# Kernel optimization log

Measured on AMD Instinct MI355X. Metric: run time of the kernel, lower is better.

## Reference

```python
import jax, jax.numpy as jnp
import numpy as np

B, S, D, H = 2, 2048, 1024, 16
HD = D // H  # 64

def _make_freqs():
    # flux-style rotation matrices: [1,1,S,HD//2,2,2]
    theta = 10000.0
    inv = 1.0 / (theta ** (np.arange(0, HD, 2, dtype=np.float32) / HD))  # [HD//2]
    pos = np.arange(S, dtype=np.float32)
    ang = pos[:, None] * inv[None, :]  # [S, HD//2]
    cos, sin = np.cos(ang), np.sin(ang)
    rot = np.stack([np.stack([cos, -sin], -1), np.stack([sin, cos], -1)], -2)  # [S,HD//2,2,2]
    return jnp.asarray(rot[None, None], dtype=jnp.float32)

def setup_inputs() -> dict:
    key = jax.random.key(0)
    ks = jax.random.split(key, 9)
    sc = 1.0 / np.sqrt(D)
    return {
        "x": jax.random.normal(ks[0], (B, S, D), jnp.float32),
        "freqs": _make_freqs(),
        "Wq": jax.random.normal(ks[1], (D, D), jnp.float32) * sc,
        "bq": jax.random.normal(ks[2], (D,), jnp.float32) * 0.01,
        "Wk": jax.random.normal(ks[3], (D, D), jnp.float32) * sc,
        "bk": jax.random.normal(ks[4], (D,), jnp.float32) * 0.01,
        "Wv": jax.random.normal(ks[5], (D, D), jnp.float32) * sc,
        "bv": jax.random.normal(ks[6], (D,), jnp.float32) * 0.01,
        "Wo": jax.random.normal(ks[7], (D, D), jnp.float32) * sc,
        "bo": jax.random.normal(ks[8], (D,), jnp.float32) * 0.01,
    }

def _apply_rope(xq, xk, freqs):
    # xq/xk: [B,H,S,HD]; freqs: [1,1,S,HD//2,2,2]
    def rot(t):
        t_ = t.reshape(*t.shape[:-1], -1, 1, 2)  # [B,H,S,HD//2,1,2]
        out = freqs[..., 0] * t_[..., 0] + freqs[..., 1] * t_[..., 1]  # [B,H,S,HD//2,2]
        return out.reshape(t.shape).astype(t.dtype)
    return rot(xq), rot(xk)

def reference(x, freqs, Wq, bq, Wk, bk, Wv, bv, Wo, bo):
    b, s, _ = x.shape
    # QKV projections (torch Linear: x @ W.T + b)
    q = (x @ Wq.T + bq).reshape(b, s, H, HD).transpose(0, 2, 1, 3)  # [B,H,S,HD]
    k = (x @ Wk.T + bk).reshape(b, s, H, HD).transpose(0, 2, 1, 3)
    v = (x @ Wv.T + bv).reshape(b, s, H, HD).transpose(0, 2, 1, 3)
    q, k = _apply_rope(q, k, freqs)
    # scaled dot product attention, no mask, no dropout
    scale = 1.0 / jnp.sqrt(jnp.asarray(HD, x.dtype))
    scores = jnp.einsum("bhqd,bhkd->bhqk", q, k) * scale
    attn = jax.nn.softmax(scores, axis=-1)
    o = jnp.einsum("bhqk,bhkd->bhqd", attn, v)  # [B,H,S,HD]
    o = o.transpose(0, 2, 1, 3).reshape(b, s, D)
    return o @ Wo.T + bo
```

## Files before the change

kernel.cpp:

```cpp
#include <hip/hip_runtime.h>
#include <cmath>

#define B_ 2
#define S_ 2048
#define D_ 1024
#define H_ 16
#define HD_ 64
#define M_ 4096

typedef __attribute__((ext_vector_type(8))) short short8;
typedef __attribute__((ext_vector_type(4))) short short4v;
typedef __attribute__((ext_vector_type(4))) float f32x4;

__device__ __forceinline__ short f2bf(float x) {
    unsigned u = __builtin_bit_cast(unsigned, x);
    u += 0x7fffu + ((u >> 16) & 1u);
    return (short)(u >> 16);
}

__device__ __forceinline__ void gload_lds16(const short* g, short* l) {
    __builtin_amdgcn_global_load_lds(
        (const __attribute__((address_space(1))) unsigned int*)g,
        (__attribute__((address_space(3))) unsigned int*)l, 16, 0, 0);
}

__global__ __launch_bounds__(256) void cast_all_kernel(
    const float* __restrict__ x,  const float* __restrict__ Wq,
    const float* __restrict__ Wk, const float* __restrict__ Wv,
    const float* __restrict__ Wo,
    short* __restrict__ xb, short* __restrict__ Wqkvb, short* __restrict__ Wob)
{
    const size_t i = (size_t)blockIdx.x * 256 + threadIdx.x;
    const float* src; short* dst; size_t off;
    if (i < 1048576)      { src = x;  dst = xb;              off = i; }
    else if (i < 1310720) { src = Wq; dst = Wqkvb;           off = i - 1048576; }
    else if (i < 1572864) { src = Wk; dst = Wqkvb + 1048576; off = i - 1310720; }
    else if (i < 1835008) { src = Wv; dst = Wqkvb + 2097152; off = i - 1572864; }
    else                  { src = Wo; dst = Wob;             off = i - 1835008; }
    float4 v = ((const float4*)src)[off];
    short4v o = { f2bf(v.x), f2bf(v.y), f2bf(v.z), f2bf(v.w) };
    ((short4v*)dst)[off] = o;
}

template<int MODE, int TM, int TN>
__global__ __launch_bounds__(256) void gemm_db(
    const short* __restrict__ A, const short* __restrict__ Bw,
    const float* __restrict__ b0p, const float* __restrict__ b1p, const float* __restrict__ b2p,
    const float* __restrict__ freqs,
    void* __restrict__ out0, void* __restrict__ out1, void* __restrict__ out2)
{
    constexpr int RT = TM / 32, CT = TN / 32;
    __shared__ __align__(16) short A0[TM*32];
    __shared__ __align__(16) short A1[TM*32];
    __shared__ __align__(16) short Bs0[TN*32];
    __shared__ __align__(16) short Bs1[TN*32];
    const int t = threadIdx.x;
    const int w = t >> 6;
    const int lane = t & 63;
    const int qd = lane >> 4, l = lane & 15;
    const int n0 = blockIdx.x * TN, m0 = blockIdx.y * TM;
    const int wr = (w >> 1) * (TM/2), wc = (w & 1) * (TN/2);
    const int srow  = lane >> 2;
    const int sslot = ((lane & 3) ^ ((lane >> 3) & 3)) * 8;
    const int rsw = (l >> 1) & 3;

    f32x4 acc[RT][CT] = {};

    auto STAGE = [&](int k0, short* As, short* Bss) {
        #pragma unroll
        for (int j = 0; j < TM/64; ++j) {
            const int r0 = (j*4 + w) * 16;
            gload_lds16(A + (size_t)(m0 + r0 + srow)*1024 + k0 + sslot, &As[r0*32]);
        }
        #pragma unroll
        for (int j = 0; j < TN/64; ++j) {
            const int r0 = (j*4 + w) * 16;
            gload_lds16(Bw + (size_t)(n0 + r0 + srow)*1024 + k0 + sslot, &Bss[r0*32]);
        }
    };

    auto COMP = [&](const short* As, const short* Bss) {
        short8 af[RT], bfr[CT];
        #pragma unroll
        for (int rt = 0; rt < RT; ++rt)
            af[rt] = *(const short8*)&As[(wr + rt*16 + l)*32 + ((qd ^ rsw) << 3)];
        #pragma unroll
        for (int ct = 0; ct < CT; ++ct)
            bfr[ct] = *(const short8*)&Bss[(wc + ct*16 + l)*32 + ((qd ^ rsw) << 3)];
        #pragma unroll
        for (int rt = 0; rt < RT; ++rt)
            #pragma unroll
            for (int ct = 0; ct < CT; ++ct)
                acc[rt][ct] = __builtin_amdgcn_mfma_f32_16x16x32_bf16(af[rt], bfr[ct], acc[rt][ct], 0, 0, 0);
    };

    STAGE(0, A0, Bs0);
    __syncthreads();
    for (int p = 0; p < 16; ++p) {
        STAGE((2*p + 1)*32, A1, Bs1);
        COMP(A0, Bs0);
        __syncthreads();
        if (p < 15)
            STAGE((2*p + 2)*32, A0, Bs0);
        COMP(A1, Bs1);
        __syncthreads();
    }

    if (MODE == 0) {
        float* out = (float*)out0;
        #pragma unroll
        for (int rt = 0; rt < RT; ++rt)
            #pragma unroll
            for (int ct = 0; ct < CT; ++ct) {
                const int n = n0 + wc + ct*16 + l;
                const float bias = b0p[n];
                #pragma unroll
                for (int r = 0; r < 4; ++r) {
                    const int m = m0 + wr + rt*16 + qd*4 + r;
                    out[(size_t)m*1024 + n] = acc[rt][ct][r] + bias;
                }
            }
    } else {
        const int sel = n0 >> 10;
        const int nb = n0 & 1023;
        const float* bias = (sel == 0) ? b0p : (sel == 1) ? b1p : b2p;
        if (sel < 2) {
            short* outg = (short*)((sel == 0) ? out0 : out1);
            #pragma unroll
            for (int rt = 0; rt < RT; ++rt)
                #pragma unroll
                for (int ct = 0; ct < CT; ++ct) {
                    const int d = nb + wc + ct*16 + l;
                    const float bsv = bias[d];
                    const int h = d >> 6, hd = d & 63;
                    #pragma unroll
                    for (int r = 0; r < 4; ++r) {
                        const int m = m0 + wr + rt*16 + qd*4 + r;
                        const int bb = m >> 11, s = m & 2047;
                        float val = acc[rt][ct][r] + bsv;
                        float pv = __shfl_xor(val, 1);
                        const float* f = freqs + (size_t)s*128 + (size_t)(hd >> 1)*4;
                        float o = (d & 1) ? (f[2]*pv + f[3]*val) : (f[0]*val + f[1]*pv);
                        outg[((size_t)(bb*16 + h)*2048 + s)*64 + hd] = f2bf(o);
                    }
                }
        } else {
            short* outv = (short*)out2;
            #pragma unroll
            for (int rt = 0; rt < RT; ++rt)
                #pragma unroll
                for (int ct = 0; ct < CT; ++ct) {
                    const int d = nb + wc + ct*16 + l;
                    const float bsv = bias[d];
                    const int h = d >> 6, hd = d & 63;
                    const int m0r = m0 + wr + rt*16 + qd*4;
                    const int bb = m0r >> 11, s0 = m0r & 2047;
                    short4v pk;
                    #pragma unroll
                    for (int r = 0; r < 4; ++r) pk[r] = f2bf(acc[rt][ct][r] + bsv);
                    *(short4v*)&outv[((size_t)(bb*16 + h)*64 + hd)*2048 + s0] = pk;
                }
        }
    }
}

__global__ __launch_bounds__(512) void attn_mfma(
    const short* __restrict__ qg, const short* __restrict__ kg,
    const short* __restrict__ vtg, short* __restrict__ og)
{
    __shared__ __align__(16) short K0[64*64];
    __shared__ __align__(16) short K1[64*64];
    __shared__ __align__(16) short V0[64*64];
    __shared__ __align__(16) short V1[64*64];
    __shared__ __align__(16) short Pb[128*64];

    const int t = threadIdx.x;
    const int w = t >> 6;
    const int lane = t & 63;
    const int qd = lane >> 4, l = lane & 15;
    const int l7 = lane & 7;
    const int q0 = blockIdx.x * 128;
    const int bh = blockIdx.y;

    const int rl  = lane >> 3;
    const int ss8 = ((lane & 7) ^ rl) << 3;

    short8 qf[2];
    const short* qb = qg + ((size_t)bh*2048 + q0 + w*16)*64;
    #pragma unroll
    for (int kf = 0; kf < 2; ++kf)
        qf[kf] = *(const short8*)&qb[l*64 + kf*32 + qd*8];

    f32x4 oacc[4] = {};
    float lsum = 0.f;

    const short* kbase = kg  + (size_t)bh*2048*64;
    const short* vbase = vtg + (size_t)bh*64*2048;
    const float SC = 0.125f * 1.44269504088896340736f;

    auto PREF = [&](int c, short* Kd, short* Vd) {
        gload_lds16(kbase + (size_t)(c*64 + w*8 + rl)*64 + ss8,   &Kd[(w*8)*64]);
        gload_lds16(vbase + (size_t)(w*8 + rl)*2048 + c*64 + ss8, &Vd[(w*8)*64]);
    };

    auto TILE = [&](const short* Kc, const short* Vc) {
        f32x4 sacc[4] = {};
        #pragma unroll
        for (int ct = 0; ct < 4; ++ct) {
            short8 k0f = *(const short8*)&Kc[(ct*16 + l)*64 + (((0 + qd) ^ l7) << 3)];
            short8 k1f = *(const short8*)&Kc[(ct*16 + l)*64 + (((4 + qd) ^ l7) << 3)];
            sacc[ct] = __builtin_amdgcn_mfma_f32_16x16x32_bf16(k0f, qf[0], sacc[ct], 0, 0, 0);
            sacc[ct] = __builtin_amdgcn_mfma_f32_16x16x32_bf16(k1f, qf[1], sacc[ct], 0, 0, 0);
        }
        #pragma unroll
        for (int ct = 0; ct < 4; ++ct) {
            float p0 = exp2f(sacc[ct][0] * SC);
            float p1 = exp2f(sacc[ct][1] * SC);
            float p2 = exp2f(sacc[ct][2] * SC);
            float p3 = exp2f(sacc[ct][3] * SC);
            lsum += (p0 + p1) + (p2 + p3);
            union { unsigned u[2]; short4v s; } cv;
            asm("v_cvt_pk_bf16_f32 %0, %1, %2" : "=v"(cv.u[0]) : "v"(p0), "v"(p1));
            asm("v_cvt_pk_bf16_f32 %0, %1, %2" : "=v"(cv.u[1]) : "v"(p2), "v"(p3));
            *(short4v*)&Pb[(w*16 + l)*64 + (((ct*32 + qd*8) ^ (l7 << 4)) >> 1)] = cv.s;
        }
        #pragma unroll
        for (int kf = 0; kf < 2; ++kf) {
            const int so = ((kf*4 + qd) ^ l7) << 3;
            short8 pa = *(const short8*)&Pb[(w*16 + l)*64 + so];
            #pragma unroll
            for (int ht = 0; ht < 4; ++ht) {
                short8 vb = *(const short8*)&Vc[(ht*16 + l)*64 + so];
                oacc[ht] = __builtin_amdgcn_mfma_f32_16x16x32_bf16(pa, vb, oacc[ht], 0, 0, 0);
            }
        }
    };

    PREF(0, K0, V0);
    __syncthreads();
    for (int p = 0; p < 16; ++p) {
        PREF(2*p + 1, K1, V1);
        TILE(K0, V0);
        __syncthreads();
        if (p < 15)
            PREF(2*p + 2, K0, V0);
        TILE(K1, V1);
        __syncthreads();
    }

    lsum += __shfl_xor(lsum, 16);
    lsum += __shfl_xor(lsum, 32);
    float inv[4];
    #pragma unroll
    for (int r = 0; r < 4; ++r)
        inv[r] = 1.0f / __shfl(lsum, qd*4 + r);

    const int bb = bh >> 4, h = bh & 15;
    #pragma unroll
    for (int ht = 0; ht < 4; ++ht)
        #pragma unroll
        for (int r = 0; r < 4; ++r) {
            const int s = q0 + w*16 + qd*4 + r;
            og[((size_t)bb*2048 + s)*1024 + h*64 + ht*16 + l] =
                f2bf(oacc[ht][r] * inv[r]);
        }
}

extern "C" void kernel_launch(void* const* d_in, const int* in_sizes, int n_in,
                              void* d_out, int out_size, void* d_ws, size_t ws_size,
                              hipStream_t stream)
{
    const float* x  = (const float*)d_in[0];
    const float* fr = (const float*)d_in[1];
    const float* Wq = (const float*)d_in[2];
    const float* bq = (const float*)d_in[3];
    const float* Wk = (const float*)d_in[4];
    const float* bk = (const float*)d_in[5];
    const float* Wv = (const float*)d_in[6];
    const float* bv = (const float*)d_in[7];
    const float* Wo = (const float*)d_in[8];
    const float* bo = (const float*)d_in[9];
    float* out = (float*)d_out;

    short* ws    = (short*)d_ws;
    short* xb    = ws;
    short* Wqkvb = xb    + 4194304;
    short* Wob   = Wqkvb + 3145728;
    short* qg    = Wob   + 1048576;
    short* kg    = qg    + 4194304;
    short* vtg   = kg    + 4194304;
    short* og    = vtg   + 4194304;

    cast_all_kernel<<<8192, 256, 0, stream>>>(x, Wq, Wk, Wv, Wo, xb, Wqkvb, Wob);
    gemm_db<1,128,128><<<dim3(24, 32), 256, 0, stream>>>(xb, Wqkvb, bq, bk, bv, fr, qg, kg, vtg);
    attn_mfma<<<dim3(16, 32), 512, 0, stream>>>(qg, kg, vtg, og);
    gemm_db<0,64,64><<<dim3(16, 64), 256, 0, stream>>>(og, Wob, bo, nullptr, nullptr, nullptr,
                                                       out, nullptr, nullptr);
}
```

Measured before the change: 247.7 us.

## Replace syncthreads with vmcnt-based waits to keep two stages in flight

The double-buffered loops in the GEMM and attention kernels now issue loads for two tiles up front. Each stage then waits with explicit s_waitcnt vmcnt(N) plus a raw barrier, so the next tile's global-to-LDS loads stay outstanding while the current tile is computed, instead of draining at every __syncthreads. The output projection GEMM tile also grows from 64x64 to 128x64, halving its grid. The hand-counted vmcnt values must match the number of loads issued per STAGE/PREF, otherwise the kernel races.

```diff
diff --git a/kernel.cpp b/kernel.cpp
--- a/kernel.cpp
+++ b/kernel.cpp
@@ -23,6 +23,15 @@
         (const __attribute__((address_space(1))) unsigned int*)g,
         (__attribute__((address_space(3))) unsigned int*)l, 16, 0, 0);
 }
+
+template<int N> __device__ __forceinline__ void vwait() {
+    if constexpr (N == 0) asm volatile("s_waitcnt vmcnt(0)" ::: "memory");
+    else if constexpr (N == 2) asm volatile("s_waitcnt vmcnt(2)" ::: "memory");
+    else if constexpr (N == 3) asm volatile("s_waitcnt vmcnt(3)" ::: "memory");
+    else if constexpr (N == 4) asm volatile("s_waitcnt vmcnt(4)" ::: "memory");
+}
+__device__ __forceinline__ void lgwait0() { asm volatile("s_waitcnt lgkmcnt(0)" ::: "memory"); }
+__device__ __forceinline__ void bar() { __builtin_amdgcn_s_barrier(); }
 
 __global__ __launch_bounds__(256) void cast_all_kernel(
     const float* __restrict__ x,  const float* __restrict__ Wq,
@@ -50,6 +59,7 @@
     void* __restrict__ out0, void* __restrict__ out1, void* __restrict__ out2)
 {
     constexpr int RT = TM / 32, CT = TN / 32;
+    constexpr int LPC = TM/64 + TN/64;
     __shared__ __align__(16) short A0[TM*32];
     __shared__ __align__(16) short A1[TM*32];
     __shared__ __align__(16) short Bs0[TN*32];
@@ -95,16 +105,21 @@
     };
 
     STAGE(0, A0, Bs0);
-    __syncthreads();
-    for (int p = 0; p < 16; ++p) {
-        STAGE((2*p + 1)*32, A1, Bs1);
+    STAGE(32, A1, Bs1);
+    for (int p = 0; p < 30; p += 2) {
+        vwait<LPC>(); bar();
         COMP(A0, Bs0);
-        __syncthreads();
-        if (p < 15)
-            STAGE((2*p + 2)*32, A0, Bs0);
+        lgwait0(); bar();
+        STAGE((p + 2)*32, A0, Bs0);
+        vwait<LPC>(); bar();
         COMP(A1, Bs1);
-        __syncthreads();
+        lgwait0(); bar();
+        STAGE((p + 3)*32, A1, Bs1);
     }
+    vwait<LPC>(); bar();
+    COMP(A0, Bs0);
+    vwait<0>(); bar();
+    COMP(A1, Bs1);
 
     if (MODE == 0) {
         float* out = (float*)out0;
@@ -237,16 +252,21 @@
     };
 
     PREF(0, K0, V0);
-    __syncthreads();
-    for (int p = 0; p < 16; ++p) {
-        PREF(2*p + 1, K1, V1);
+    PREF(1, K1, V1);
+    for (int p = 0; p < 30; p += 2) {
+        vwait<2>(); bar();
         TILE(K0, V0);
-        __syncthreads();
-        if (p < 15)
-            PREF(2*p + 2, K0, V0);
+        lgwait0(); bar();
+        PREF(p + 2, K0, V0);
+        vwait<2>(); bar();
         TILE(K1, V1);
-        __syncthreads();
+        lgwait0(); bar();
+        PREF(p + 3, K1, V1);
     }
+    vwait<2>(); bar();
+    TILE(K0, V0);
+    vwait<0>(); bar();
+    TILE(K1, V1);
 
     lsum += __shfl_xor(lsum, 16);
     lsum += __shfl_xor(lsum, 32);
@@ -294,6 +314,6 @@
     cast_all_kernel<<<8192, 256, 0, stream>>>(x, Wq, Wk, Wv, Wo, xb, Wqkvb, Wob);
     gemm_db<1,128,128><<<dim3(24, 32), 256, 0, stream>>>(xb, Wqkvb, bq, bk, bv, fr, qg, kg, vtg);
     attn_mfma<<<dim3(16, 32), 512, 0, stream>>>(qg, kg, vtg, og);
-    gemm_db<0,64,64><<<dim3(16, 64), 256, 0, stream>>>(og, Wob, bo, nullptr, nullptr, nullptr,
-                                                       out, nullptr, nullptr);
-}
+    gemm_db<0,128,64><<<dim3(16, 32), 256, 0, stream>>>(og, Wob, bo, nullptr, nullptr, nullptr,
+                                                        out, nullptr, nullptr);
+}
```

Result: no change. 251.8 us (+1.6%).

## Double K-step per stage in GEMMs with 8-way XOR swizzle and explicit waits

Applied to the files above, without the earlier changes.

Each pipeline stage of both projection GEMMs now covers a K chunk of 64 instead of 32, which halves the number of barrier phases. The LDS layout uses rows of 64 elements with an 8-slot XOR swizzle. Syncthreads is replaced by an explicit vmcnt(0) wait plus s_barrier. The output projection tile grows from 64x64 to 128x64, which improves operand reuse but halves the grid size and doubles LDS use per block.

```diff
diff --git a/kernel.cpp b/kernel.cpp
--- a/kernel.cpp
+++ b/kernel.cpp
@@ -23,6 +23,9 @@
         (const __attribute__((address_space(1))) unsigned int*)g,
         (__attribute__((address_space(3))) unsigned int*)l, 16, 0, 0);
 }
+
+__device__ __forceinline__ void vwait0() { asm volatile("s_waitcnt vmcnt(0)" ::: "memory"); }
+__device__ __forceinline__ void bar()    { __builtin_amdgcn_s_barrier(); }
 
 __global__ __launch_bounds__(256) void cast_all_kernel(
     const float* __restrict__ x,  const float* __restrict__ Wq,
@@ -43,67 +46,70 @@
 }
 
 template<int MODE, int TM, int TN>
-__global__ __launch_bounds__(256) void gemm_db(
+__global__ __launch_bounds__(256) void gemm_2ph(
     const short* __restrict__ A, const short* __restrict__ Bw,
     const float* __restrict__ b0p, const float* __restrict__ b1p, const float* __restrict__ b2p,
     const float* __restrict__ freqs,
     void* __restrict__ out0, void* __restrict__ out1, void* __restrict__ out2)
 {
     constexpr int RT = TM / 32, CT = TN / 32;
-    __shared__ __align__(16) short A0[TM*32];
-    __shared__ __align__(16) short A1[TM*32];
-    __shared__ __align__(16) short Bs0[TN*32];
-    __shared__ __align__(16) short Bs1[TN*32];
+    __shared__ __align__(16) short A0[TM*64];
+    __shared__ __align__(16) short A1[TM*64];
+    __shared__ __align__(16) short Bs0[TN*64];
+    __shared__ __align__(16) short Bs1[TN*64];
     const int t = threadIdx.x;
     const int w = t >> 6;
     const int lane = t & 63;
     const int qd = lane >> 4, l = lane & 15;
+    const int l7 = lane & 7;
     const int n0 = blockIdx.x * TN, m0 = blockIdx.y * TM;
     const int wr = (w >> 1) * (TM/2), wc = (w & 1) * (TN/2);
-    const int srow  = lane >> 2;
-    const int sslot = ((lane & 3) ^ ((lane >> 3) & 3)) * 8;
-    const int rsw = (l >> 1) & 3;
+    const int rl  = lane >> 3;
+    const int ss8 = ((lane & 7) ^ rl) << 3;
 
     f32x4 acc[RT][CT] = {};
 
     auto STAGE = [&](int k0, short* As, short* Bss) {
         #pragma unroll
-        for (int j = 0; j < TM/64; ++j) {
-            const int r0 = (j*4 + w) * 16;
-            gload_lds16(A + (size_t)(m0 + r0 + srow)*1024 + k0 + sslot, &As[r0*32]);
-        }
-        #pragma unroll
-        for (int j = 0; j < TN/64; ++j) {
-            const int r0 = (j*4 + w) * 16;
-            gload_lds16(Bw + (size_t)(n0 + r0 + srow)*1024 + k0 + sslot, &Bss[r0*32]);
+        for (int j = 0; j < TM/32; ++j) {
+            const int r0 = (j*4 + w) * 8;
+            gload_lds16(A + (size_t)(m0 + r0 + rl)*1024 + k0 + ss8, &As[r0*64]);
+        }
+        #pragma unroll
+        for (int j = 0; j < TN/32; ++j) {
+            const int r0 = (j*4 + w) * 8;
+            gload_lds16(Bw + (size_t)(n0 + r0 + rl)*1024 + k0 + ss8, &Bss[r0*64]);
         }
     };
 
     auto COMP = [&](const short* As, const short* Bss) {
-        short8 af[RT], bfr[CT];
-        #pragma unroll
-        for (int rt = 0; rt < RT; ++rt)
-            af[rt] = *(const short8*)&As[(wr + rt*16 + l)*32 + ((qd ^ rsw) << 3)];
-        #pragma unroll
-        for (int ct = 0; ct < CT; ++ct)
-            bfr[ct] = *(const short8*)&Bss[(wc + ct*16 + l)*32 + ((qd ^ rsw) << 3)];
-        #pragma unroll
-        for (int rt = 0; rt < RT; ++rt)
+        #pragma unroll
+        for (int kk = 0; kk < 2; ++kk) {
+            short8 af[RT], bfr[CT];
+            #pragma unroll
+            for (int rt = 0; rt < RT; ++rt)
+                af[rt] = *(const short8*)&As[(wr + rt*16 + l)*64 + (((kk*4 + qd) ^ l7) << 3)];
             #pragma unroll
             for (int ct = 0; ct < CT; ++ct)
-                acc[rt][ct] = __builtin_amdgcn_mfma_f32_16x16x32_bf16(af[rt], bfr[ct], acc[rt][ct], 0, 0, 0);
+                bfr[ct] = *(const short8*)&Bss[(wc + ct*16 + l)*64 + (((kk*4 + qd) ^ l7) << 3)];
+            #pragma unroll
+            for (int rt = 0; rt < RT; ++rt)
+                #pragma unroll
+                for (int ct = 0; ct < CT; ++ct)
+                    acc[rt][ct] = __builtin_amdgcn_mfma_f32_16x16x32_bf16(af[rt], bfr[ct], acc[rt][ct], 0, 0, 0);
+        }
     };
 
     STAGE(0, A0, Bs0);
-    __syncthreads();
-    for (int p = 0; p < 16; ++p) {
-        STAGE((2*p + 1)*32, A1, Bs1);
+    vwait0(); bar();
+    for (int p = 0; p < 16; p += 2) {
+        STAGE((p + 1)*64, A1, Bs1);
         COMP(A0, Bs0);
-        __syncthreads();
-        if (p < 15)
-            STAGE((2*p + 2)*32, A0, Bs0);
+        vwait0(); bar();
+        if (p + 2 < 16)
+            STAGE((p + 2)*64, A0, Bs0);
         COMP(A1, Bs1);
-        __syncthreads();
+        vwait0(); bar();
     }
 
     if (MODE == 0) {
@@ -292,8 +298,8 @@
     short* og    = vtg   + 4194304;
 
     cast_all_kernel<<<8192, 256, 0, stream>>>(x, Wq, Wk, Wv, Wo, xb, Wqkvb, Wob);
-    gemm_db<1,128,128><<<dim3(24, 32), 256, 0, stream>>>(xb, Wqkvb, bq, bk, bv, fr, qg, kg, vtg);
+    gemm_2ph<1,128,128><<<dim3(24, 32), 256, 0, stream>>>(xb, Wqkvb, bq, bk, bv, fr, qg, kg, vtg);
     attn_mfma<<<dim3(16, 32), 512, 0, stream>>>(qg, kg, vtg, og);
-    gemm_db<0,64,64><<<dim3(16, 64), 256, 0, stream>>>(og, Wob, bo, nullptr, nullptr, nullptr,
-                                                       out, nullptr, nullptr);
-}
+    gemm_2ph<0,128,64><<<dim3(16, 32), 256, 0, stream>>>(og, Wob, bo, nullptr, nullptr, nullptr,
+                                                         out, nullptr, nullptr);
+}
```

Result: slower. 278.5 us (+12.4%).

## Triple-buffer GEMM LDS staging with explicit vmcnt waits and barriers

Applied to the files above, without the earlier changes.

Replaces the double-buffered GEMM main loop with a three-stage LDS ring. Each step waits only on the oldest outstanding global-to-LDS loads (s_waitcnt vmcnt) and issues a raw s_barrier, instead of a full __syncthreads drain. This keeps two K-chunks of loads in flight while the MFMA work runs, hiding more global memory latency. The cost is 50% more shared memory per block, which may reduce occupancy. It also relies on hand-counted wait values, which must match the number of load instructions each stage issues.

```diff
diff --git a/kernel.cpp b/kernel.cpp
--- a/kernel.cpp
+++ b/kernel.cpp
@@ -23,6 +23,17 @@
         (const __attribute__((address_space(1))) unsigned int*)g,
         (__attribute__((address_space(3))) unsigned int*)l, 16, 0, 0);
 }
+
+template<int N> __device__ __forceinline__ void vwait() {
+    if constexpr (N == 0) asm volatile("s_waitcnt vmcnt(0)" ::: "memory");
+    else if constexpr (N == 2) asm volatile("s_waitcnt vmcnt(2)" ::: "memory");
+    else if constexpr (N == 3) asm volatile("s_waitcnt vmcnt(3)" ::: "memory");
+    else if constexpr (N == 4) asm volatile("s_waitcnt vmcnt(4)" ::: "memory");
+    else if constexpr (N == 6) asm volatile("s_waitcnt vmcnt(6)" ::: "memory");
+    else if constexpr (N == 8) asm volatile("s_waitcnt vmcnt(8)" ::: "memory");
+}
+__device__ __forceinline__ void lgwait0() { asm volatile("s_waitcnt lgkmcnt(0)" ::: "memory"); }
+__device__ __forceinline__ void bar() { __builtin_amdgcn_s_barrier(); }
 
 __global__ __launch_bounds__(256) void cast_all_kernel(
     const float* __restrict__ x,  const float* __restrict__ Wq,
@@ -43,17 +54,20 @@
 }
 
 template<int MODE, int TM, int TN>
-__global__ __launch_bounds__(256) void gemm_db(
+__global__ __launch_bounds__(256) void gemm_d3(
     const short* __restrict__ A, const short* __restrict__ Bw,
     const float* __restrict__ b0p, const float* __restrict__ b1p, const float* __restrict__ b2p,
     const float* __restrict__ freqs,
     void* __restrict__ out0, void* __restrict__ out1, void* __restrict__ out2)
 {
     constexpr int RT = TM / 32, CT = TN / 32;
+    constexpr int LPC = TM/64 + TN/64;
     __shared__ __align__(16) short A0[TM*32];
     __shared__ __align__(16) short A1[TM*32];
-    __shared__ __align__(16) short Bs0[TN*32];
-    __shared__ __align__(16) short Bs1[TN*32];
+    __shared__ __align__(16) short A2[TM*32];
+    __shared__ __align__(16) short B0[TN*32];
+    __shared__ __align__(16) short B1[TN*32];
+    __shared__ __align__(16) short B2[TN*32];
     const int t = threadIdx.x;
     const int w = t >> 6;
     const int lane = t & 63;
@@ -66,7 +80,8 @@
 
     f32x4 acc[RT][CT] = {};
 
-    auto STAGE = [&](int k0, short* As, short* Bss) {
+    auto STAGE = [&](int c, short* As, short* Bss) {
+        const int k0 = c * 32;
         #pragma unroll
         for (int j = 0; j < TM/64; ++j) {
             const int r0 = (j*4 + w) * 16;
@@ -94,17 +109,37 @@
                 acc[rt][ct] = __builtin_amdgcn_mfma_f32_16x16x32_bf16(af[rt], bfr[ct], acc[rt][ct], 0, 0, 0);
     };
 
-    STAGE(0, A0, Bs0);
-    __syncthreads();
-    for (int p = 0; p < 16; ++p) {
-        STAGE((2*p + 1)*32, A1, Bs1);
-        COMP(A0, Bs0);
-        __syncthreads();
-        if (p < 15)
-            STAGE((2*p + 2)*32, A0, Bs0);
-        COMP(A1, Bs1);
-        __syncthreads();
+    STAGE(0, A0, B0);
+    STAGE(1, A1, B1);
+    STAGE(2, A2, B2);
+    for (int p = 0; p <= 24; p += 3) {
+        vwait<2*LPC>(); bar();
+        COMP(A0, B0);
+        lgwait0(); bar();
+        STAGE(p + 3, A0, B0);
+        vwait<2*LPC>(); bar();
+        COMP(A1, B1);
+        lgwait0(); bar();
+        STAGE(p + 4, A1, B1);
+        vwait<2*LPC>(); bar();
+        COMP(A2, B2);
+        lgwait0(); bar();
+        STAGE(p + 5, A2, B2);
     }
+    vwait<2*LPC>(); bar();
+    COMP(A0, B0);
+    lgwait0(); bar();
+    STAGE(30, A0, B0);
+    vwait<2*LPC>(); bar();
+    COMP(A1, B1);
+    lgwait0(); bar();
+    STAGE(31, A1, B1);
+    vwait<2*LPC>(); bar();
+    COMP(A2, B2);
+    vwait<LPC>(); bar();
+    COMP(A0, B0);
+    vwait<0>(); bar();
+    COMP(A1, B1);
 
     if (MODE == 0) {
         float* out = (float*)out0;
@@ -292,8 +327,8 @@
     short* og    = vtg   + 4194304;
 
     cast_all_kernel<<<8192, 256, 0, stream>>>(x, Wq, Wk, Wv, Wo, xb, Wqkvb, Wob);
-    gemm_db<1,128,128><<<dim3(24, 32), 256, 0, stream>>>(xb, Wqkvb, bq, bk, bv, fr, qg, kg, vtg);
+    gemm_d3<1,128,128><<<dim3(24, 32), 256, 0, stream>>>(xb, Wqkvb, bq, bk, bv, fr, qg, kg, vtg);
     attn_mfma<<<dim3(16, 32), 512, 0, stream>>>(qg, kg, vtg, og);
-    gemm_db<0,64,64><<<dim3(16, 64), 256, 0, stream>>>(og, Wob, bo, nullptr, nullptr, nullptr,
+    gemm_d3<0,64,64><<<dim3(16, 64), 256, 0, stream>>>(og, Wob, bo, nullptr, nullptr, nullptr,
                                                        out, nullptr, nullptr);
 }
```

Result: faster. 241.5 us (-2.5%).
